# Kernel tuning notes

Hardware: AMD Instinct MI355X
Metric: run time of the kernel (lower is better)

## Reference

```python
import jax, jax.numpy as jnp
import numpy as np

EMB_SIZE = 768
BLOCK_SIZE = 64
NUM_CLASS = 97
N = 4096
NUM_BLOCKS = EMB_SIZE // BLOCK_SIZE  # 12


def setup_inputs() -> dict:
    key = jax.random.key(0)
    k1, k2, k3 = jax.random.split(key, 3)
    head_embeddings = jax.random.normal(k1, (N, EMB_SIZE), dtype=jnp.float32)
    tail_embeddings = jax.random.normal(k2, (N, EMB_SIZE), dtype=jnp.float32)
    # xavier_uniform for [NUM_CLASS, EMB_SIZE*BLOCK_SIZE]
    fan_in = EMB_SIZE * BLOCK_SIZE
    fan_out = NUM_CLASS
    bound = float(np.sqrt(6.0 / (fan_in + fan_out)))
    W = jax.random.uniform(k3, (NUM_CLASS, EMB_SIZE * BLOCK_SIZE), dtype=jnp.float32,
                           minval=-bound, maxval=bound)
    b = jnp.full((NUM_CLASS,), 0.1, dtype=jnp.float32)
    return {"head_embeddings": head_embeddings, "tail_embeddings": tail_embeddings,
            "W": W, "b": b}


def reference(head_embeddings, tail_embeddings, W, b):
    n = head_embeddings.shape[0]
    b1 = head_embeddings.reshape(n, NUM_BLOCKS, BLOCK_SIZE)  # [N, K, S]
    b2 = tail_embeddings.reshape(n, NUM_BLOCKS, BLOCK_SIZE)  # [N, K, S]
    # block-wise outer product: [N, K, S, S] -> [N, K*S*S]
    bl = jnp.einsum('nki,nkj->nkij', b1, b2).reshape(n, EMB_SIZE * BLOCK_SIZE)
    logits = bl @ W.T + b  # [N, NUM_CLASS]
    return logits
```

## Files before the change

### kernel.cpp

```cpp
#include <hip/hip_runtime.h>
#include <hip/hip_bf16.h>
#include <stdint.h>

#define NROWS 4096
#define NCLS  97
#define EMB   768
#define KTOT  49152
#define OUT_ELEMS (NROWS * NCLS)
#define E_ELEMS  (NROWS * EMB)
#define NK32  (KTOT / 32)
#define WT_BYTES ((size_t)NK32 * 128 * 64)
#define EB_BYTES ((size_t)E_ELEMS * 2)

typedef __attribute__((ext_vector_type(8)))  short short8;
typedef __attribute__((ext_vector_type(4)))  float floatx4;
typedef __bf16 bf16x2 __attribute__((ext_vector_type(2)));
typedef __bf16 bf16x8 __attribute__((ext_vector_type(8)));

__device__ __forceinline__ uint32_t pkmul(uint32_t a, uint32_t b) {
  bf16x2 x = __builtin_bit_cast(bf16x2, a);
  bf16x2 y = __builtin_bit_cast(bf16x2, b);
  bf16x2 r = x * y;
  return __builtin_bit_cast(uint32_t, r);
}

__device__ __forceinline__ uint4 cvt8(float4 a, float4 b) {
  bf16x8 v;
  v[0] = (__bf16)a.x; v[1] = (__bf16)a.y; v[2] = (__bf16)a.z; v[3] = (__bf16)a.w;
  v[4] = (__bf16)b.x; v[5] = (__bf16)b.y; v[6] = (__bf16)b.z; v[7] = (__bf16)b.w;
  return __builtin_bit_cast(uint4, v);
}

__global__ void prep(const float* __restrict__ W,
                     const float* __restrict__ b1,
                     const float* __restrict__ b2,
                     uint4* __restrict__ wt,
                     uint4* __restrict__ b1b,
                     uint4* __restrict__ b2b,
                     int nmax)
{
  const int nwt = NK32 * 128 * 4;
  const int nE8 = E_ELEMS / 8;
  int t = blockIdx.x * blockDim.x + threadIdx.x;
  if (t >= nmax) return;
  if (t < nwt) {
    int eo = t & 3;
    int c  = (t >> 2) & 127;
    int kc = t >> 9;
    uint4 v = uint4{0u, 0u, 0u, 0u};
    if (c < NCLS) {
      const float4* p = (const float4*)(W + (size_t)c * KTOT + kc * 32 + eo * 8);
      v = cvt8(p[0], p[1]);
    }
    wt[t] = v;
  } else if (t < nwt + nE8) {
    int i = t - nwt;
    const float4* p = (const float4*)b1 + (size_t)2 * i;
    b1b[i] = cvt8(p[0], p[1]);
  } else {
    int i = t - nwt - nE8;
    const float4* p = (const float4*)b2 + (size_t)2 * i;
    b2b[i] = cvt8(p[0], p[1]);
  }
}

template<bool BMIR>
__global__ __launch_bounds__(256, 2)
void bilinear_main(const void* __restrict__ b1p,
                   const void* __restrict__ b2p,
                   const char* __restrict__ Wt,
                   const float* __restrict__ biasg,
                   float* __restrict__ P,
                   float* __restrict__ outd,
                   int klen)
{
  const int tid  = threadIdx.x;
  const int w    = tid >> 6;
  const int l    = tid & 63;
  const int l15  = l & 15;
  const int quad = l >> 4;
  const int mhalf = w & 1;
  const int chalf = w >> 1;
  const int bm = blockIdx.y;
  const int k0 = blockIdx.x * klen;

  int nrow[4];
#pragma unroll
  for (int rt = 0; rt < 4; ++rt) nrow[rt] = bm * 128 + mhalf * 64 + rt * 16 + l15;

  const char* wtl = Wt + (size_t)(k0 >> 5) * 8192
                       + (chalf * 64 + l15) * 64 + quad * 16;

  floatx4 acc[4][4];
#pragma unroll
  for (int rt = 0; rt < 4; ++rt)
#pragma unroll
    for (int ct = 0; ct < 4; ++ct)
      acc[rt][ct] = floatx4{0.f, 0.f, 0.f, 0.f};

  uint4 b2c[4][2];
  uint4 b1c[4];
  int cur_k = -1;
  const int nwin = klen >> 6;

  for (int gwin = 0; gwin < nwin; gwin += 8) {
    const int kap0 = k0 + (gwin << 6);
    const int kblk = kap0 >> 12;
    const int i0   = (kap0 >> 6) & 63;
    if (kblk != cur_k) {
      cur_k = kblk;
#pragma unroll
      for (int rt = 0; rt < 4; ++rt)
#pragma unroll
        for (int kh = 0; kh < 2; ++kh) {
          if (BMIR) {
            b2c[rt][kh] = *(const uint4*)((const char*)b2p +
                            (size_t)nrow[rt] * 1536 + kblk * 128 + kh * 64 + quad * 16);
          } else {
            const float* p = (const float*)b2p + (size_t)nrow[rt] * EMB +
                             kblk * 64 + kh * 32 + quad * 8;
            b2c[rt][kh] = cvt8(((const float4*)p)[0], ((const float4*)p)[1]);
          }
        }
    }
#pragma unroll
    for (int rt = 0; rt < 4; ++rt) {
      if (BMIR) {
        b1c[rt] = *(const uint4*)((const char*)b1p +
                     (size_t)nrow[rt] * 1536 + kblk * 128 + i0 * 2);
      } else {
        const float* p = (const float*)b1p + (size_t)nrow[rt] * EMB + kblk * 64 + i0;
        b1c[rt] = cvt8(((const float4*)p)[0], ((const float4*)p)[1]);
      }
    }

#pragma unroll
    for (int ii = 0; ii < 8; ++ii) {
      const char* pw = wtl + (size_t)(gwin + ii) * 16384;

      uint32_t s2[4];
#pragma unroll
      for (int rt = 0; rt < 4; ++rt) {
        uint32_t d = (&b1c[rt].x)[ii >> 1];
        uint32_t h = (ii & 1) ? (d >> 16) : (d & 0xffffu);
        s2[rt] = h | (h << 16);
      }

#pragma unroll
      for (int kh = 0; kh < 2; ++kh) {
        short8 wf[4];
#pragma unroll
        for (int ct = 0; ct < 4; ++ct)
          wf[ct] = __builtin_bit_cast(short8,
                     *(const uint4*)(pw + kh * 8192 + ct * 1024));
        uint4 afr[4];
#pragma unroll
        for (int rt = 0; rt < 4; ++rt) {
          afr[rt].x = pkmul(s2[rt], b2c[rt][kh].x);
          afr[rt].y = pkmul(s2[rt], b2c[rt][kh].y);
          afr[rt].z = pkmul(s2[rt], b2c[rt][kh].z);
          afr[rt].w = pkmul(s2[rt], b2c[rt][kh].w);
        }
#pragma unroll
        for (int rt = 0; rt < 4; ++rt) {
          short8 af = __builtin_bit_cast(short8, afr[rt]);
#pragma unroll
          for (int ct = 0; ct < 4; ++ct)
            acc[rt][ct] = __builtin_amdgcn_mfma_f32_16x16x32_bf16(
                              af, wf[ct], acc[rt][ct], 0, 0, 0);
        }
      }
    }
  }

  if (P) {
    float* Pb = P + (size_t)blockIdx.x * OUT_ELEMS;
#pragma unroll
    for (int rt = 0; rt < 4; ++rt)
#pragma unroll
      for (int ct = 0; ct < 4; ++ct) {
        const int c = chalf * 64 + ct * 16 + l15;
        if (c < NCLS) {
#pragma unroll
          for (int r = 0; r < 4; ++r) {
            const int row = bm * 128 + mhalf * 64 + rt * 16 + quad * 4 + r;
            Pb[(size_t)row * NCLS + c] = acc[rt][ct][r];
          }
        }
      }
  } else {
#pragma unroll
    for (int rt = 0; rt < 4; ++rt)
#pragma unroll
      for (int ct = 0; ct < 4; ++ct) {
        const int c = chalf * 64 + ct * 16 + l15;
        if (c < NCLS) {
          const float bv = biasg[c];
#pragma unroll
          for (int r = 0; r < 4; ++r) {
            const int row = bm * 128 + mhalf * 64 + rt * 16 + quad * 4 + r;
            outd[(size_t)row * NCLS + c] = acc[rt][ct][r] + bv;
          }
        }
      }
  }
}

__global__ void reduce_bias(const float* __restrict__ P,
                            const float* __restrict__ biasg,
                            float* __restrict__ out, int KS)
{
  int i = blockIdx.x * blockDim.x + threadIdx.x;
  const int n4 = OUT_ELEMS / 4;
  if (i >= n4) return;
  int c0 = (i * 4) % NCLS;
  int c1 = c0 + 1 == NCLS ? 0 : c0 + 1;
  int c2 = c1 + 1 == NCLS ? 0 : c1 + 1;
  int c3 = c2 + 1 == NCLS ? 0 : c2 + 1;
  float4 s;
  s.x = biasg[c0]; s.y = biasg[c1]; s.z = biasg[c2]; s.w = biasg[c3];
  const float4* P4 = (const float4*)P;
  for (int t = 0; t < KS; ++t) {
    float4 v = P4[(size_t)t * n4 + i];
    s.x += v.x; s.y += v.y; s.z += v.z; s.w += v.w;
  }
  ((float4*)out)[i] = s;
}

extern "C" void kernel_launch(void* const* d_in, const int* in_sizes, int n_in,
                              void* d_out, int out_size, void* d_ws, size_t ws_size,
                              hipStream_t stream) {
  const float* b1f = (const float*)d_in[0];
  const float* b2f = (const float*)d_in[1];
  const float* Wf  = (const float*)d_in[2];
  const float* bbf = (const float*)d_in[3];
  float* out = (float*)d_out;

  const size_t resv_full = WT_BYTES + 2 * EB_BYTES;
  const size_t slice     = (size_t)OUT_ELEMS * 4;
  static const int cands[] = {16, 12, 8, 6, 4, 3, 2, 1};

  int KS = 0; bool bmir = false;
  for (int i = 0; i < 8; ++i)
    if (resv_full + (size_t)cands[i] * slice <= ws_size) { KS = cands[i]; bmir = true; break; }
  if (!bmir)
    for (int i = 0; i < 8; ++i)
      if (WT_BYTES + (size_t)cands[i] * slice <= ws_size) { KS = cands[i]; break; }

  uint4* Wt  = (uint4*)d_ws;
  uint4* b1b = (uint4*)((char*)d_ws + WT_BYTES);
  uint4* b2b = (uint4*)((char*)d_ws + WT_BYTES + EB_BYTES);
  const int nwt = NK32 * 128 * 4;
  const int nE8 = E_ELEMS / 8;
  const int nprep = bmir ? (nwt + 2 * nE8) : nwt;

  prep<<<(nprep + 255) / 256, 256, 0, stream>>>(Wf, b1f, b2f, Wt, b1b, b2b, nprep);

  if (KS > 0) {
    float* P = (float*)((char*)d_ws + (bmir ? resv_full : WT_BYTES));
    if (bmir)
      bilinear_main<true><<<dim3(KS, 32), 256, 0, stream>>>(
          (const void*)b1b, (const void*)b2b, (const char*)Wt, bbf, P, nullptr, KTOT / KS);
    else
      bilinear_main<false><<<dim3(KS, 32), 256, 0, stream>>>(
          (const void*)b1f, (const void*)b2f, (const char*)Wt, bbf, P, nullptr, KTOT / KS);
    reduce_bias<<<(OUT_ELEMS / 4 + 255) / 256, 256, 0, stream>>>(P, bbf, out, KS);
  } else {
    bilinear_main<false><<<dim3(1, 32), 256, 0, stream>>>(
        (const void*)b1f, (const void*)b2f, (const char*)Wt, bbf, nullptr, out, KTOT);
  }
}
```

Measured before the change: 153.8 us.

## Drop embedding bf16 mirror, raise split-K to 32, remap blocks by XCD

The prep kernel no longer converts head and tail embeddings to bf16; the main kernel always reads fp32 embeddings and converts them in registers. Split-K candidates now go up to 32 slices, and the 2D grid becomes a 1D grid. When the slice count is a multiple of 8, each group of 8 consecutive block IDs covers 8 K-slices of the same row tile, intended to place distinct W slices on different XCDs while sharing embedding rows. This saves the mirror prep pass and adds more K parallelism. In exchange it doubles the embedding read bytes in the main loop and enlarges the partial buffer and the reduction.

```diff
diff --git a/kernel.cpp b/kernel.cpp
--- a/kernel.cpp
+++ b/kernel.cpp
@@ -7,10 +7,8 @@
 #define EMB   768
 #define KTOT  49152
 #define OUT_ELEMS (NROWS * NCLS)
-#define E_ELEMS  (NROWS * EMB)
 #define NK32  (KTOT / 32)
 #define WT_BYTES ((size_t)NK32 * 128 * 64)
-#define EB_BYTES ((size_t)E_ELEMS * 2)
 
 typedef __attribute__((ext_vector_type(8)))  short short8;
 typedef __attribute__((ext_vector_type(4)))  float floatx4;
@@ -31,48 +29,30 @@
   return __builtin_bit_cast(uint4, v);
 }
 
-__global__ void prep(const float* __restrict__ W,
-                     const float* __restrict__ b1,
-                     const float* __restrict__ b2,
-                     uint4* __restrict__ wt,
-                     uint4* __restrict__ b1b,
-                     uint4* __restrict__ b2b,
-                     int nmax)
+__global__ void prep_wt(const float* __restrict__ W, uint4* __restrict__ wt)
 {
   const int nwt = NK32 * 128 * 4;
-  const int nE8 = E_ELEMS / 8;
   int t = blockIdx.x * blockDim.x + threadIdx.x;
-  if (t >= nmax) return;
-  if (t < nwt) {
-    int eo = t & 3;
-    int c  = (t >> 2) & 127;
-    int kc = t >> 9;
-    uint4 v = uint4{0u, 0u, 0u, 0u};
-    if (c < NCLS) {
-      const float4* p = (const float4*)(W + (size_t)c * KTOT + kc * 32 + eo * 8);
-      v = cvt8(p[0], p[1]);
-    }
-    wt[t] = v;
-  } else if (t < nwt + nE8) {
-    int i = t - nwt;
-    const float4* p = (const float4*)b1 + (size_t)2 * i;
-    b1b[i] = cvt8(p[0], p[1]);
-  } else {
-    int i = t - nwt - nE8;
-    const float4* p = (const float4*)b2 + (size_t)2 * i;
-    b2b[i] = cvt8(p[0], p[1]);
-  }
-}
-
-template<bool BMIR>
+  if (t >= nwt) return;
+  int eo = t & 3;
+  int c  = (t >> 2) & 127;
+  int kc = t >> 9;
+  uint4 v = uint4{0u, 0u, 0u, 0u};
+  if (c < NCLS) {
+    const float4* p = (const float4*)(W + (size_t)c * KTOT + kc * 32 + eo * 8);
+    v = cvt8(p[0], p[1]);
+  }
+  wt[t] = v;
+}
+
 __global__ __launch_bounds__(256, 2)
-void bilinear_main(const void* __restrict__ b1p,
-                   const void* __restrict__ b2p,
+void bilinear_main(const float* __restrict__ b1g,
+                   const float* __restrict__ b2g,
                    const char* __restrict__ Wt,
                    const float* __restrict__ biasg,
                    float* __restrict__ P,
                    float* __restrict__ outd,
-                   int klen)
+                   int klen, int nslice, int G)
 {
   const int tid  = threadIdx.x;
   const int w    = tid >> 6;
@@ -81,8 +61,12 @@
   const int quad = l >> 4;
   const int mhalf = w & 1;
   const int chalf = w >> 1;
-  const int bm = blockIdx.y;
-  const int k0 = blockIdx.x * klen;
+
+  const int n = blockIdx.x;
+  int s, bm;
+  if (G > 0) { s = (n & 7) + 8 * ((n >> 3) % G); bm = (n >> 3) / G; }
+  else       { s = n % nslice;                   bm = n / nslice; }
+  const int k0 = s * klen;
 
   int nrow[4];
 #pragma unroll
@@ -113,25 +97,15 @@
       for (int rt = 0; rt < 4; ++rt)
 #pragma unroll
         for (int kh = 0; kh < 2; ++kh) {
-          if (BMIR) {
-            b2c[rt][kh] = *(const uint4*)((const char*)b2p +
-                            (size_t)nrow[rt] * 1536 + kblk * 128 + kh * 64 + quad * 16);
-          } else {
-            const float* p = (const float*)b2p + (size_t)nrow[rt] * EMB +
-                             kblk * 64 + kh * 32 + quad * 8;
-            b2c[rt][kh] = cvt8(((const float4*)p)[0], ((const float4*)p)[1]);
-          }
+          const float* p = b2g + (size_t)nrow[rt] * EMB +
+                           kblk * 64 + kh * 32 + quad * 8;
+          b2c[rt][kh] = cvt8(((const float4*)p)[0], ((const float4*)p)[1]);
         }
     }
 #pragma unroll
     for (int rt = 0; rt < 4; ++rt) {
-      if (BMIR) {
-        b1c[rt] = *(const uint4*)((const char*)b1p +
-                     (size_t)nrow[rt] * 1536 + kblk * 128 + i0 * 2);
-      } else {
-        const float* p = (const float*)b1p + (size_t)nrow[rt] * EMB + kblk * 64 + i0;
-        b1c[rt] = cvt8(((const float4*)p)[0], ((const float4*)p)[1]);
-      }
+      const float* p = b1g + (size_t)nrow[rt] * EMB + kblk * 64 + i0;
+      b1c[rt] = cvt8(((const float4*)p)[0], ((const float4*)p)[1]);
     }
 
 #pragma unroll
@@ -174,7 +148,7 @@
   }
 
   if (P) {
-    float* Pb = P + (size_t)blockIdx.x * OUT_ELEMS;
+    float* Pb = P + (size_t)s * OUT_ELEMS;
 #pragma unroll
     for (int rt = 0; rt < 4; ++rt)
 #pragma unroll
@@ -236,37 +210,24 @@
   const float* bbf = (const float*)d_in[3];
   float* out = (float*)d_out;
 
-  const size_t resv_full = WT_BYTES + 2 * EB_BYTES;
-  const size_t slice     = (size_t)OUT_ELEMS * 4;
-  static const int cands[] = {16, 12, 8, 6, 4, 3, 2, 1};
-
-  int KS = 0; bool bmir = false;
-  for (int i = 0; i < 8; ++i)
-    if (resv_full + (size_t)cands[i] * slice <= ws_size) { KS = cands[i]; bmir = true; break; }
-  if (!bmir)
-    for (int i = 0; i < 8; ++i)
-      if (WT_BYTES + (size_t)cands[i] * slice <= ws_size) { KS = cands[i]; break; }
-
-  uint4* Wt  = (uint4*)d_ws;
-  uint4* b1b = (uint4*)((char*)d_ws + WT_BYTES);
-  uint4* b2b = (uint4*)((char*)d_ws + WT_BYTES + EB_BYTES);
+  const size_t slice = (size_t)OUT_ELEMS * 4;
+  static const int cands[] = {32, 24, 16, 12, 8, 6, 4, 3, 2, 1};
+  int KS = 0;
+  for (int i = 0; i < 10; ++i)
+    if (WT_BYTES + (size_t)cands[i] * slice <= ws_size) { KS = cands[i]; break; }
+
+  uint4* Wt = (uint4*)d_ws;
   const int nwt = NK32 * 128 * 4;
-  const int nE8 = E_ELEMS / 8;
-  const int nprep = bmir ? (nwt + 2 * nE8) : nwt;
-
-  prep<<<(nprep + 255) / 256, 256, 0, stream>>>(Wf, b1f, b2f, Wt, b1b, b2b, nprep);
+  prep_wt<<<(nwt + 255) / 256, 256, 0, stream>>>(Wf, Wt);
 
   if (KS > 0) {
-    float* P = (float*)((char*)d_ws + (bmir ? resv_full : WT_BYTES));
-    if (bmir)
-      bilinear_main<true><<<dim3(KS, 32), 256, 0, stream>>>(
-          (const void*)b1b, (const void*)b2b, (const char*)Wt, bbf, P, nullptr, KTOT / KS);
-    else
-      bilinear_main<false><<<dim3(KS, 32), 256, 0, stream>>>(
-          (const void*)b1f, (const void*)b2f, (const char*)Wt, bbf, P, nullptr, KTOT / KS);
+    float* P = (float*)((char*)d_ws + WT_BYTES);
+    const int G = (KS % 8 == 0) ? KS / 8 : 0;
+    bilinear_main<<<dim3(KS * 32), 256, 0, stream>>>(
+        b1f, b2f, (const char*)Wt, bbf, P, nullptr, KTOT / KS, KS, G);
     reduce_bias<<<(OUT_ELEMS / 4 + 255) / 256, 256, 0, stream>>>(P, bbf, out, KS);
   } else {
-    bilinear_main<false><<<dim3(1, 32), 256, 0, stream>>>(
-        (const void*)b1f, (const void*)b2f, (const char*)Wt, bbf, nullptr, out, KTOT);
-  }
-}
+    bilinear_main<<<dim3(32), 256, 0, stream>>>(
+        b1f, b2f, (const char*)Wt, bbf, nullptr, out, KTOT, 1, 0);
+  }
+}
```

New measurement: 172.8 us. 1.12x slower.

## Switch bilinear GEMM to 32x32x16 MFMA with per-wave 32-class column tiles

Applied to the files above, without the earlier changes.

Replaces the 16x16x32 bf16 MFMA tiling (each wave 64 rows x 64 classes) with 32x32x16 MFMA, where each of four waves owns 32 classes across all 128 rows of the block. The aim is fewer W fragment loads per MFMA and better MFMA throughput per instruction, with the A-operand outer-product fragments built once per row tile. The output mapping is recomputed for the 32x32 accumulator layout. The fourth wave mostly covers padded classes beyond 97, which wastes part of the compute and may leave that wave's work unbalanced.

```diff
diff --git a/kernel.cpp b/kernel.cpp
--- a/kernel.cpp
+++ b/kernel.cpp
@@ -13,7 +13,7 @@
 #define EB_BYTES ((size_t)E_ELEMS * 2)
 
 typedef __attribute__((ext_vector_type(8)))  short short8;
-typedef __attribute__((ext_vector_type(4)))  float floatx4;
+typedef __attribute__((ext_vector_type(16))) float floatx16;
 typedef __bf16 bf16x2 __attribute__((ext_vector_type(2)));
 typedef __bf16 bf16x8 __attribute__((ext_vector_type(8)));
 
@@ -74,52 +74,50 @@
                    float* __restrict__ outd,
                    int klen)
 {
-  const int tid  = threadIdx.x;
-  const int w    = tid >> 6;
-  const int l    = tid & 63;
-  const int l15  = l & 15;
-  const int quad = l >> 4;
-  const int mhalf = w & 1;
-  const int chalf = w >> 1;
-  const int bm = blockIdx.y;
-  const int k0 = blockIdx.x * klen;
+  const int tid = threadIdx.x;
+  const int w   = tid >> 6;
+  const int l   = tid & 63;
+  const int l31 = l & 31;
+  const int q8  = l >> 5;
+  const int s   = blockIdx.x;
+  const int bm  = blockIdx.y;
+  const int k0  = s * klen;
+  const int win0 = k0 >> 6;
+  const int nwin = klen >> 6;
 
   int nrow[4];
 #pragma unroll
-  for (int rt = 0; rt < 4; ++rt) nrow[rt] = bm * 128 + mhalf * 64 + rt * 16 + l15;
-
-  const char* wtl = Wt + (size_t)(k0 >> 5) * 8192
-                       + (chalf * 64 + l15) * 64 + quad * 16;
-
-  floatx4 acc[4][4];
+  for (int rt = 0; rt < 4; ++rt) nrow[rt] = bm * 128 + rt * 32 + l31;
+
+  const char* wtl = Wt + (w * 32 + l31) * 64 + q8 * 16;
+
+  floatx16 acc[4];
 #pragma unroll
   for (int rt = 0; rt < 4; ++rt)
 #pragma unroll
-    for (int ct = 0; ct < 4; ++ct)
-      acc[rt][ct] = floatx4{0.f, 0.f, 0.f, 0.f};
-
-  uint4 b2c[4][2];
+    for (int r = 0; r < 16; ++r) acc[rt][r] = 0.0f;
+
+  uint4 b2c[4][4];
   uint4 b1c[4];
   int cur_k = -1;
-  const int nwin = klen >> 6;
-
-  for (int gwin = 0; gwin < nwin; gwin += 8) {
-    const int kap0 = k0 + (gwin << 6);
-    const int kblk = kap0 >> 12;
-    const int i0   = (kap0 >> 6) & 63;
+
+  for (int wg = 0; wg < nwin; wg += 8) {
+    const int win  = win0 + wg;
+    const int kblk = win >> 6;
+    const int i0   = win & 63;
     if (kblk != cur_k) {
       cur_k = kblk;
 #pragma unroll
       for (int rt = 0; rt < 4; ++rt)
 #pragma unroll
-        for (int kh = 0; kh < 2; ++kh) {
+        for (int ks = 0; ks < 4; ++ks) {
           if (BMIR) {
-            b2c[rt][kh] = *(const uint4*)((const char*)b2p +
-                            (size_t)nrow[rt] * 1536 + kblk * 128 + kh * 64 + quad * 16);
+            b2c[rt][ks] = *(const uint4*)((const char*)b2p +
+                            (size_t)nrow[rt] * 1536 + kblk * 128 + ks * 32 + q8 * 16);
           } else {
             const float* p = (const float*)b2p + (size_t)nrow[rt] * EMB +
-                             kblk * 64 + kh * 32 + quad * 8;
-            b2c[rt][kh] = cvt8(((const float4*)p)[0], ((const float4*)p)[1]);
+                             kblk * 64 + ks * 16 + q8 * 8;
+            b2c[rt][ks] = cvt8(((const float4*)p)[0], ((const float4*)p)[1]);
           }
         }
     }
@@ -136,7 +134,7 @@
 
 #pragma unroll
     for (int ii = 0; ii < 8; ++ii) {
-      const char* pw = wtl + (size_t)(gwin + ii) * 16384;
+      const char* pw = wtl + (size_t)(win + ii) * 16384;
 
       uint32_t s2[4];
 #pragma unroll
@@ -147,62 +145,46 @@
       }
 
 #pragma unroll
-      for (int kh = 0; kh < 2; ++kh) {
-        short8 wf[4];
-#pragma unroll
-        for (int ct = 0; ct < 4; ++ct)
-          wf[ct] = __builtin_bit_cast(short8,
-                     *(const uint4*)(pw + kh * 8192 + ct * 1024));
-        uint4 afr[4];
+      for (int ks = 0; ks < 4; ++ks) {
+        short8 wf = __builtin_bit_cast(short8,
+                      *(const uint4*)(pw + (ks >> 1) * 8192 + (ks & 1) * 32));
 #pragma unroll
         for (int rt = 0; rt < 4; ++rt) {
-          afr[rt].x = pkmul(s2[rt], b2c[rt][kh].x);
-          afr[rt].y = pkmul(s2[rt], b2c[rt][kh].y);
-          afr[rt].z = pkmul(s2[rt], b2c[rt][kh].z);
-          afr[rt].w = pkmul(s2[rt], b2c[rt][kh].w);
-        }
-#pragma unroll
-        for (int rt = 0; rt < 4; ++rt) {
-          short8 af = __builtin_bit_cast(short8, afr[rt]);
-#pragma unroll
-          for (int ct = 0; ct < 4; ++ct)
-            acc[rt][ct] = __builtin_amdgcn_mfma_f32_16x16x32_bf16(
-                              af, wf[ct], acc[rt][ct], 0, 0, 0);
+          uint4 afr;
+          afr.x = pkmul(s2[rt], b2c[rt][ks].x);
+          afr.y = pkmul(s2[rt], b2c[rt][ks].y);
+          afr.z = pkmul(s2[rt], b2c[rt][ks].z);
+          afr.w = pkmul(s2[rt], b2c[rt][ks].w);
+          short8 af = __builtin_bit_cast(short8, afr);
+          acc[rt] = __builtin_amdgcn_mfma_f32_32x32x16_bf16(af, wf, acc[rt], 0, 0, 0);
         }
       }
     }
   }
 
+  const int c = w * 32 + l31;
   if (P) {
-    float* Pb = P + (size_t)blockIdx.x * OUT_ELEMS;
-#pragma unroll
-    for (int rt = 0; rt < 4; ++rt)
-#pragma unroll
-      for (int ct = 0; ct < 4; ++ct) {
-        const int c = chalf * 64 + ct * 16 + l15;
-        if (c < NCLS) {
-#pragma unroll
-          for (int r = 0; r < 4; ++r) {
-            const int row = bm * 128 + mhalf * 64 + rt * 16 + quad * 4 + r;
-            Pb[(size_t)row * NCLS + c] = acc[rt][ct][r];
-          }
-        }
-      }
+    float* Pb = P + (size_t)s * OUT_ELEMS;
+    if (c < NCLS) {
+#pragma unroll
+      for (int rt = 0; rt < 4; ++rt)
+#pragma unroll
+        for (int r = 0; r < 16; ++r) {
+          const int row = bm * 128 + rt * 32 + (r & 3) + 8 * (r >> 2) + 4 * q8;
+          Pb[(size_t)row * NCLS + c] = acc[rt][r];
+        }
+    }
   } else {
-#pragma unroll
-    for (int rt = 0; rt < 4; ++rt)
-#pragma unroll
-      for (int ct = 0; ct < 4; ++ct) {
-        const int c = chalf * 64 + ct * 16 + l15;
-        if (c < NCLS) {
-          const float bv = biasg[c];
-#pragma unroll
-          for (int r = 0; r < 4; ++r) {
-            const int row = bm * 128 + mhalf * 64 + rt * 16 + quad * 4 + r;
-            outd[(size_t)row * NCLS + c] = acc[rt][ct][r] + bv;
-          }
-        }
-      }
+    if (c < NCLS) {
+      const float bv = biasg[c];
+#pragma unroll
+      for (int rt = 0; rt < 4; ++rt)
+#pragma unroll
+        for (int r = 0; r < 16; ++r) {
+          const int row = bm * 128 + rt * 32 + (r & 3) + 8 * (r >> 2) + 4 * q8;
+          outd[(size_t)row * NCLS + c] = acc[rt][r] + bv;
+        }
+    }
   }
 }
 
@@ -253,7 +235,6 @@
   const int nwt = NK32 * 128 * 4;
   const int nE8 = E_ELEMS / 8;
   const int nprep = bmir ? (nwt + 2 * nE8) : nwt;
-
   prep<<<(nprep + 255) / 256, 256, 0, stream>>>(Wf, b1f, b2f, Wt, b1b, b2b, nprep);
 
   if (KS > 0) {
```

New measurement: 197.0 us. 1.28x slower.
